# Performance work log

Measured on AMD Instinct MI355X. Metric: run time of the kernel, lower is better.

## Reference

```python
import jax, jax.numpy as jnp
import numpy as np

D = 256       # d_model
H = 8         # nhead
W = 2048      # num windows (single drop level)
T = 64        # max_tokens per window (drop_info['num_sampled_tokens'][dl])
FILL = 48
N = W * FILL  # total voxels


def setup_inputs() -> dict:
    key = jax.random.key(0)
    k0, k1, k2, k3 = jax.random.split(key, 4)
    voxel_feat = jax.random.normal(k0, (N, D), jnp.float32)
    pos_embed = jax.random.normal(k1, (N, D), jnp.float32)
    # nn.MultiheadAttention params: packed in_proj [3D, D] and out_proj [D, D]
    in_proj_w = jax.random.normal(k2, (3 * D, D), jnp.float32) * (1.0 / np.sqrt(D))
    in_proj_b = jnp.zeros((3 * D,), jnp.float32)
    out_proj_w = jax.random.normal(k3, (D, D), jnp.float32) * (1.0 / np.sqrt(D))
    out_proj_b = jnp.zeros((D,), jnp.float32)
    # each voxel assigned a (window, in-window-slot) pair; slots unique per window
    window_idx = (jnp.arange(N) // FILL).astype(jnp.int32)
    slot_idx = (jnp.arange(N) % FILL).astype(jnp.int32)
    return {
        'voxel_feat': voxel_feat, 'pos_embed': pos_embed,
        'in_proj_w': in_proj_w, 'in_proj_b': in_proj_b,
        'out_proj_w': out_proj_w, 'out_proj_b': out_proj_b,
        'window_idx': window_idx, 'slot_idx': slot_idx,
        'num_windows': W, 'max_tokens': T,
    }


def reference(voxel_feat, pos_embed, in_proj_w, in_proj_b, out_proj_w, out_proj_b,
              window_idx, slot_idx, num_windows, max_tokens):
    Dm = voxel_feat.shape[-1]
    hd = Dm // H  # head dim
    P = num_windows * max_tokens  # padded token count
    valid = window_idx.astype(jnp.int32) * max_tokens + slot_idx.astype(jnp.int32)

    # scatter voxels into padded dense windows
    feat = jnp.zeros((P, Dm), voxel_feat.dtype).at[valid].set(voxel_feat)
    pos = jnp.ones((P, Dm), voxel_feat.dtype).at[valid].set(pos_embed)
    kmask = jnp.zeros((P,), bool).at[valid].set(True).reshape(num_windows, max_tokens)  # True = valid key
    feat = feat.reshape(num_windows, max_tokens, Dm)
    pos = pos.reshape(num_windows, max_tokens, Dm)

    # MHA: q = k = feat + pos, v = feat (torch nn.MultiheadAttention math)
    Wq, Wk, Wv = jnp.split(in_proj_w, 3, axis=0)
    bq, bk, bv = jnp.split(in_proj_b, 3, axis=0)
    qk_in = feat + pos
    q = (qk_in @ Wq.T + bq).reshape(num_windows, max_tokens, H, hd)
    k = (qk_in @ Wk.T + bk).reshape(num_windows, max_tokens, H, hd)
    v = (feat @ Wv.T + bv).reshape(num_windows, max_tokens, H, hd)

    scale = 1.0 / np.sqrt(hd)
    scores = jnp.einsum('wqhd,wkhd->whqk', q, k) * scale  # [W, H, T, T]
    scores = jnp.where(kmask[:, None, None, :], scores, -jnp.inf)  # key_padding_mask
    attn = jax.nn.softmax(scores, axis=-1)
    out = jnp.einsum('whqk,wkhd->wqhd', attn, v).reshape(P, Dm)
    out = out @ out_proj_w.T + out_proj_b

    # gather valid tokens back to per-voxel output (padded rows dropped, as in original)
    return out[valid]
```

## Files before the change

kernel.cpp:

```cpp
#include <hip/hip_runtime.h>

#define DD   256
#define HH   8
#define TT   64
#define WW   2048

typedef unsigned short u16;
typedef __attribute__((ext_vector_type(8))) __bf16 bf8_t;
typedef __attribute__((ext_vector_type(4))) float  f32x4;

__device__ __forceinline__ u16 f2bf(float x) {
  union { float f; unsigned u; } c; c.f = x;
  unsigned r = c.u + 0x7FFFu + ((c.u >> 16) & 1u);
  return (u16)(r >> 16);
}
__device__ __forceinline__ float bf2f(u16 x) {
  union { unsigned u; float f; } c; c.u = ((unsigned)x) << 16; return c.f;
}
__device__ __forceinline__ int pack2(float a, float b) {
  return (int)((unsigned)f2bf(a) | ((unsigned)f2bf(b) << 16));
}

__global__ void prep_weights(const float* __restrict__ inw, const float* __restrict__ outw,
                             u16* __restrict__ wq, u16* __restrict__ wo) {
  int i = blockIdx.x * blockDim.x + threadIdx.x;
  if (i < 768 * 256) wq[i] = f2bf(inw[i]);
  if (i < 256 * 256) wo[i] = f2bf(outw[i]);
}

__global__ void build_slots(const int* __restrict__ widx, const int* __restrict__ sidx,
                            int* __restrict__ wslots, int n) {
  int i = blockIdx.x * blockDim.x + threadIdx.x;
  if (i < n) wslots[widx[i] * TT + sidx[i]] = i;
}

__global__ __launch_bounds__(512) void fused_attn(
    const float* __restrict__ feat, const float* __restrict__ pos,
    const u16* __restrict__ wqkv,
    const u16* __restrict__ wout,
    const float* __restrict__ inb, const float* __restrict__ outb,
    const int* __restrict__ wslots, float* __restrict__ out) {

  __shared__ int tl[TT];
  __shared__ u16 bufX[TT * 264];
  __shared__ u16 bufY[DD * 72];

  const int t    = threadIdx.x;
  const int h    = t >> 6;
  const int lane = t & 63;
  const int g    = lane >> 4;
  const int l16  = lane & 15;
  const int w    = blockIdx.x;

  if (t < TT) tl[t] = wslots[w * TT + t];
  __syncthreads();

  const f32x4 zf = {0.f, 0.f, 0.f, 0.f};
  const int stok = t >> 3;
  const int seg  = t & 7;
  const int srow = tl[stok];

  if (srow >= 0) {
    const float4* fp = (const float4*)(feat + (size_t)srow * DD + seg * 32);
    float4 f[8];
#pragma unroll
    for (int j = 0; j < 8; ++j) f[j] = fp[j];
#pragma unroll
    for (int c = 0; c < 4; ++c) {
      union { u16 u[8]; bf8_t v; } r;
#pragma unroll
      for (int j = 0; j < 8; ++j) r.u[j] = f2bf(((const float*)f)[c * 8 + j]);
      *(bf8_t*)&bufX[stok * 264 + seg * 32 + c * 8] = r.v;
    }
  } else {
    union { u16 u[8]; bf8_t v; } z;
#pragma unroll
    for (int j = 0; j < 8; ++j) z.u[j] = 0;
#pragma unroll
    for (int c = 0; c < 4; ++c)
      *(bf8_t*)&bufX[stok * 264 + seg * 32 + c * 8] = z.v;
  }
  __syncthreads();

  f32x4 va[2][4];
#pragma unroll
  for (int md = 0; md < 2; ++md)
#pragma unroll
    for (int nt = 0; nt < 4; ++nt) va[md][nt] = zf;

  for (int kc = 0; kc < 4; ++kc) {
    bf8_t bx[4][2];
#pragma unroll
    for (int nt = 0; nt < 4; ++nt)
#pragma unroll
      for (int ks = 0; ks < 2; ++ks)
        bx[nt][ks] = *(const bf8_t*)&bufX[(nt * 16 + l16) * 264 + kc * 64 + ks * 32 + g * 8];
#pragma unroll
    for (int ks = 0; ks < 2; ++ks) {
      const int kb = kc * 64 + ks * 32 + g * 8;
#pragma unroll
      for (int md = 0; md < 2; ++md) {
        bf8_t awv = *(const bf8_t*)(wqkv + (size_t)(512 + h * 32 + md * 16 + l16) * DD + kb);
#pragma unroll
        for (int nt = 0; nt < 4; ++nt)
          va[md][nt] = __builtin_amdgcn_mfma_f32_16x16x32_bf16(awv, bx[nt][ks], va[md][nt], 0, 0, 0);
      }
    }
  }
  __syncthreads();

  if (srow >= 0) {
    const float4* pp = (const float4*)(pos + (size_t)srow * DD + seg * 32);
    float4 p[8];
#pragma unroll
    for (int j = 0; j < 8; ++j) p[j] = pp[j];
#pragma unroll
    for (int c = 0; c < 4; ++c) {
      union { u16 u[8]; bf8_t v; } xb, r;
      xb.v = *(const bf8_t*)&bufX[stok * 264 + seg * 32 + c * 8];
#pragma unroll
      for (int j = 0; j < 8; ++j)
        r.u[j] = f2bf(bf2f(xb.u[j]) + ((const float*)p)[c * 8 + j]);
      *(bf8_t*)&bufX[stok * 264 + seg * 32 + c * 8] = r.v;
    }
  }
  __syncthreads();

  f32x4 qa[4][2], ka[4][2];
#pragma unroll
  for (int mt = 0; mt < 4; ++mt)
#pragma unroll
    for (int nt = 0; nt < 2; ++nt) { qa[mt][nt] = zf; ka[mt][nt] = zf; }

  for (int kc = 0; kc < 4; ++kc) {
    bf8_t ax[4][2];
#pragma unroll
    for (int mt = 0; mt < 4; ++mt)
#pragma unroll
      for (int ks = 0; ks < 2; ++ks)
        ax[mt][ks] = *(const bf8_t*)&bufX[(mt * 16 + l16) * 264 + kc * 64 + ks * 32 + g * 8];
#pragma unroll
    for (int ks = 0; ks < 2; ++ks) {
      const int kb = kc * 64 + ks * 32 + g * 8;
#pragma unroll
      for (int nt = 0; nt < 2; ++nt) {
        bf8_t bwq = *(const bf8_t*)(wqkv + (size_t)(h * 32 + nt * 16 + l16) * DD + kb);
#pragma unroll
        for (int mt = 0; mt < 4; ++mt)
          qa[mt][nt] = __builtin_amdgcn_mfma_f32_16x16x32_bf16(ax[mt][ks], bwq, qa[mt][nt], 0, 0, 0);
        bf8_t bwk = *(const bf8_t*)(wqkv + (size_t)(256 + h * 32 + nt * 16 + l16) * DD + kb);
#pragma unroll
        for (int mt = 0; mt < 4; ++mt)
          ka[mt][nt] = __builtin_amdgcn_mfma_f32_16x16x32_bf16(ax[mt][ks], bwk, ka[mt][nt], 0, 0, 0);
      }
    }
  }
  __syncthreads();

#pragma unroll
  for (int nt = 0; nt < 2; ++nt) {
    float bq = inb[h * 32 + nt * 16 + l16];
    float bk = inb[256 + h * 32 + nt * 16 + l16];
#pragma unroll
    for (int mt = 0; mt < 4; ++mt)
#pragma unroll
      for (int r = 0; r < 4; ++r) {
        bufX[(mt * 16 + 4 * g + r) * 264 + h * 32 + nt * 16 + l16] = f2bf(qa[mt][nt][r] + bq);
        bufY[(mt * 16 + 4 * g + r) * 264 + h * 32 + nt * 16 + l16] = f2bf(ka[mt][nt][r] + bk);
      }
  }
  __syncthreads();

  bf8_t akf[4], bqf[4];
#pragma unroll
  for (int mt = 0; mt < 4; ++mt) akf[mt] = *(const bf8_t*)&bufY[(mt * 16 + l16) * 264 + h * 32 + g * 8];
#pragma unroll
  for (int nt = 0; nt < 4; ++nt) bqf[nt] = *(const bf8_t*)&bufX[(nt * 16 + l16) * 264 + h * 32 + g * 8];

  f32x4 sa[4][4];
#pragma unroll
  for (int mt = 0; mt < 4; ++mt)
#pragma unroll
    for (int nt = 0; nt < 4; ++nt)
      sa[mt][nt] = __builtin_amdgcn_mfma_f32_16x16x32_bf16(akf[mt], bqf[nt], zf, 0, 0, 0);

  __syncthreads();

#pragma unroll
  for (int md = 0; md < 2; ++md)
#pragma unroll
    for (int r = 0; r < 4; ++r) {
      float bv = inb[512 + h * 32 + md * 16 + 4 * g + r];
#pragma unroll
      for (int nt = 0; nt < 4; ++nt)
        bufY[(h * 32 + md * 16 + 4 * g + r) * 72 + nt * 16 + l16] = f2bf(va[md][nt][r] + bv);
    }

  bool vm[4][4];
#pragma unroll
  for (int mt = 0; mt < 4; ++mt)
#pragma unroll
    for (int r = 0; r < 4; ++r) vm[mt][r] = (tl[mt * 16 + 4 * g + r] >= 0);

  const float scale = 0.17677669529663687f;
  int pk[4][4][2];
#pragma unroll
  for (int nt = 0; nt < 4; ++nt) {
    float sv[4][4];
    float m = -3e38f;
#pragma unroll
    for (int mt = 0; mt < 4; ++mt)
#pragma unroll
      for (int r = 0; r < 4; ++r) {
        float s = vm[mt][r] ? sa[mt][nt][r] * scale : -3e38f;
        sv[mt][r] = s;
        m = fmaxf(m, s);
      }
    m = fmaxf(m, __shfl_xor(m, 16, 64));
    m = fmaxf(m, __shfl_xor(m, 32, 64));
    float sum = 0.f;
#pragma unroll
    for (int mt = 0; mt < 4; ++mt)
#pragma unroll
      for (int r = 0; r < 4; ++r) {
        float p = vm[mt][r] ? __expf(sv[mt][r] - m) : 0.f;
        sv[mt][r] = p;
        sum += p;
      }
    sum += __shfl_xor(sum, 16, 64);
    sum += __shfl_xor(sum, 32, 64);
    float inv = sum > 0.f ? 1.f / sum : 0.f;
#pragma unroll
    for (int mt = 0; mt < 4; ++mt)
#pragma unroll
      for (int rp = 0; rp < 2; ++rp)
        pk[mt][nt][rp] = pack2(sv[mt][2 * rp] * inv, sv[mt][2 * rp + 1] * inv);
  }

  bf8_t avf[2][2];
#pragma unroll
  for (int md = 0; md < 2; ++md)
#pragma unroll
    for (int kk = 0; kk < 2; ++kk)
      avf[md][kk] = *(const bf8_t*)&bufY[(h * 32 + md * 16 + l16) * 72 + kk * 32 + g * 8];

  f32x4 oa[2][4];
#pragma unroll
  for (int md = 0; md < 2; ++md)
#pragma unroll
    for (int nt = 0; nt < 4; ++nt) oa[md][nt] = zf;

#pragma unroll
  for (int kk = 0; kk < 2; ++kk) {
#pragma unroll
    for (int nt = 0; nt < 4; ++nt) {
      union { int wd[4]; bf8_t v; } bu;
#pragma unroll
      for (int wd = 0; wd < 4; ++wd) {
        int src = l16 + 16 * (2 * (g & 1) + (wd >> 1));
        int lo = __shfl(pk[2 * kk + 0][nt][wd & 1], src, 64);
        int hi = __shfl(pk[2 * kk + 1][nt][wd & 1], src, 64);
        bu.wd[wd] = (g & 2) ? hi : lo;
      }
#pragma unroll
      for (int md = 0; md < 2; ++md)
        oa[md][nt] = __builtin_amdgcn_mfma_f32_16x16x32_bf16(avf[md][kk], bu.v, oa[md][nt], 0, 0, 0);
    }
  }

#pragma unroll
  for (int md = 0; md < 2; ++md)
#pragma unroll
    for (int nt = 0; nt < 4; ++nt) {
      union { int wd[2]; } pw;
      pw.wd[0] = pack2(oa[md][nt][0], oa[md][nt][1]);
      pw.wd[1] = pack2(oa[md][nt][2], oa[md][nt][3]);
      *(int2*)&bufX[(nt * 16 + l16) * 264 + h * 32 + md * 16 + 4 * g] = make_int2(pw.wd[0], pw.wd[1]);
    }
  __syncthreads();

  f32x4 fa[4][2];
#pragma unroll
  for (int mt = 0; mt < 4; ++mt)
#pragma unroll
    for (int nt = 0; nt < 2; ++nt) fa[mt][nt] = zf;

#pragma unroll
  for (int kk = 0; kk < 8; ++kk) {
    bf8_t aa[4];
#pragma unroll
    for (int mt = 0; mt < 4; ++mt)
      aa[mt] = *(const bf8_t*)&bufX[(mt * 16 + l16) * 264 + kk * 32 + g * 8];
#pragma unroll
    for (int nt = 0; nt < 2; ++nt) {
      bf8_t bw = *(const bf8_t*)(wout + (size_t)(h * 32 + nt * 16 + l16) * DD + kk * 32 + g * 8);
#pragma unroll
      for (int mt = 0; mt < 4; ++mt)
        fa[mt][nt] = __builtin_amdgcn_mfma_f32_16x16x32_bf16(aa[mt], bw, fa[mt][nt], 0, 0, 0);
    }
  }

#pragma unroll
  for (int nt = 0; nt < 2; ++nt) {
    float ob = outb[h * 32 + nt * 16 + l16];
#pragma unroll
    for (int mt = 0; mt < 4; ++mt)
#pragma unroll
      for (int r = 0; r < 4; ++r) {
        int tok = mt * 16 + 4 * g + r;
        int row = tl[tok];
        if (row >= 0)
          out[(size_t)row * DD + h * 32 + nt * 16 + l16] = fa[mt][nt][r] + ob;
      }
  }
}

extern "C" void kernel_launch(void* const* d_in, const int* in_sizes, int n_in,
                              void* d_out, int out_size, void* d_ws, size_t ws_size,
                              hipStream_t stream) {
  (void)n_in; (void)out_size; (void)ws_size;
  const float* feat = (const float*)d_in[0];
  const float* pos  = (const float*)d_in[1];
  const float* inw  = (const float*)d_in[2];
  const float* inb  = (const float*)d_in[3];
  const float* outw = (const float*)d_in[4];
  const float* outb = (const float*)d_in[5];
  const int*   widx = (const int*)d_in[6];
  const int*   sidx = (const int*)d_in[7];
  const int N = in_sizes[0] / DD;

  char* ws = (char*)d_ws;
  u16* wqkv   = (u16*)ws;
  u16* wout   = (u16*)(ws + 393216);
  int* wslots = (int*)(ws + 393216 + 131072);

  hipMemsetAsync(wslots, 0xFF, WW * TT * sizeof(int), stream);
  prep_weights<<<768, 256, 0, stream>>>(inw, outw, wqkv, wout);
  build_slots<<<(N + 255) / 256, 256, 0, stream>>>(widx, sidx, wslots, N);
  fused_attn<<<WW, 512, 0, stream>>>(feat, pos, wqkv, wout, inb, outb, wslots, (float*)d_out);
}
```

Before: 255.7 us.

## Process eight windows per block with register prefetch of next window's inputs

Each block now loops over eight consecutive windows instead of one. While the current window computes, the next window's feature and position rows and its slot indices are loaded into registers, with double-buffered slot tables in shared memory. Launch bounds are raised to request two blocks per CU. The aim is to hide global-load latency and cut per-block launch overhead. The cost is more register pressure and only 256 blocks, which may under-fill the device's CUs and lengthen the tail.

Result: slower. 324.4 us (+26.8%).

```diff
diff --git a/kernel.cpp b/kernel.cpp
--- a/kernel.cpp
+++ b/kernel.cpp
@@ -4,6 +4,8 @@
 #define HH   8
 #define TT   64
 #define WW   2048
+#define WPB  8
+#define NBLK (WW / WPB)
 
 typedef unsigned short u16;
 typedef __attribute__((ext_vector_type(8))) __bf16 bf8_t;
@@ -34,14 +36,14 @@
   if (i < n) wslots[widx[i] * TT + sidx[i]] = i;
 }
 
-__global__ __launch_bounds__(512) void fused_attn(
+__global__ __launch_bounds__(512, 2) void fused_attn(
     const float* __restrict__ feat, const float* __restrict__ pos,
     const u16* __restrict__ wqkv,
     const u16* __restrict__ wout,
     const float* __restrict__ inb, const float* __restrict__ outb,
     const int* __restrict__ wslots, float* __restrict__ out) {
 
-  __shared__ int tl[TT];
+  __shared__ int tl2[2][TT];
   __shared__ u16 bufX[TT * 264];
   __shared__ u16 bufY[DD * 72];
 
@@ -50,268 +52,292 @@
   const int lane = t & 63;
   const int g    = lane >> 4;
   const int l16  = lane & 15;
-  const int w    = blockIdx.x;
-
-  if (t < TT) tl[t] = wslots[w * TT + t];
+  const int base = blockIdx.x * WPB;
+
+  const int stok  = t >> 3;
+  const int seg   = t & 7;
+  const int tslot = t & 63;
+
+  const f32x4 zf = {0.f, 0.f, 0.f, 0.f};
+
+  int srow_cur = wslots[base * TT + stok];
+  {
+    int tl0 = wslots[base * TT + tslot];
+    if (t < TT) tl2[0][t] = tl0;
+  }
+  float4 fr[8], pr[8];
+  if (srow_cur >= 0) {
+    const float4* fp = (const float4*)(feat + (size_t)srow_cur * DD + seg * 32);
+    const float4* pp = (const float4*)(pos  + (size_t)srow_cur * DD + seg * 32);
+#pragma unroll
+    for (int j = 0; j < 8; ++j) { fr[j] = fp[j]; pr[j] = pp[j]; }
+  }
+  int srowN = wslots[(base + 1) * TT + stok];
+  int tlN   = wslots[(base + 1) * TT + tslot];
   __syncthreads();
 
-  const f32x4 zf = {0.f, 0.f, 0.f, 0.f};
-  const int stok = t >> 3;
-  const int seg  = t & 7;
-  const int srow = tl[stok];
-
-  if (srow >= 0) {
-    const float4* fp = (const float4*)(feat + (size_t)srow * DD + seg * 32);
-    float4 f[8];
-#pragma unroll
-    for (int j = 0; j < 8; ++j) f[j] = fp[j];
-#pragma unroll
-    for (int c = 0; c < 4; ++c) {
-      union { u16 u[8]; bf8_t v; } r;
-#pragma unroll
-      for (int j = 0; j < 8; ++j) r.u[j] = f2bf(((const float*)f)[c * 8 + j]);
-      *(bf8_t*)&bufX[stok * 264 + seg * 32 + c * 8] = r.v;
-    }
-  } else {
-    union { u16 u[8]; bf8_t v; } z;
-#pragma unroll
-    for (int j = 0; j < 8; ++j) z.u[j] = 0;
-#pragma unroll
-    for (int c = 0; c < 4; ++c)
-      *(bf8_t*)&bufX[stok * 264 + seg * 32 + c * 8] = z.v;
-  }
-  __syncthreads();
-
-  f32x4 va[2][4];
-#pragma unroll
-  for (int md = 0; md < 2; ++md)
-#pragma unroll
-    for (int nt = 0; nt < 4; ++nt) va[md][nt] = zf;
-
-  for (int kc = 0; kc < 4; ++kc) {
-    bf8_t bx[4][2];
-#pragma unroll
-    for (int nt = 0; nt < 4; ++nt)
-#pragma unroll
-      for (int ks = 0; ks < 2; ++ks)
-        bx[nt][ks] = *(const bf8_t*)&bufX[(nt * 16 + l16) * 264 + kc * 64 + ks * 32 + g * 8];
-#pragma unroll
-    for (int ks = 0; ks < 2; ++ks) {
-      const int kb = kc * 64 + ks * 32 + g * 8;
-#pragma unroll
-      for (int md = 0; md < 2; ++md) {
-        bf8_t awv = *(const bf8_t*)(wqkv + (size_t)(512 + h * 32 + md * 16 + l16) * DD + kb);
+#pragma unroll 1
+  for (int wi = 0; wi < WPB; ++wi) {
+    const int cb = wi & 1, nb = cb ^ 1;
+
+    if (srow_cur >= 0) {
+#pragma unroll
+      for (int c = 0; c < 4; ++c) {
+        union { u16 u[8]; bf8_t v; } r;
+#pragma unroll
+        for (int j = 0; j < 8; ++j) r.u[j] = f2bf(((const float*)fr)[c * 8 + j]);
+        *(bf8_t*)&bufX[stok * 264 + seg * 32 + c * 8] = r.v;
+      }
+    } else {
+      union { u16 u[8]; bf8_t v; } z;
+#pragma unroll
+      for (int j = 0; j < 8; ++j) z.u[j] = 0;
+#pragma unroll
+      for (int c = 0; c < 4; ++c)
+        *(bf8_t*)&bufX[stok * 264 + seg * 32 + c * 8] = z.v;
+    }
+    if (t < TT && wi + 1 < WPB) tl2[nb][t] = tlN;
+    if (wi + 1 < WPB && srowN >= 0) {
+      const float4* fp = (const float4*)(feat + (size_t)srowN * DD + seg * 32);
+#pragma unroll
+      for (int j = 0; j < 8; ++j) fr[j] = fp[j];
+    }
+    if (wi + 2 < WPB) tlN = wslots[(base + wi + 2) * TT + tslot];
+    __syncthreads();
+
+    f32x4 va[2][4];
+#pragma unroll
+    for (int md = 0; md < 2; ++md)
+#pragma unroll
+      for (int nt = 0; nt < 4; ++nt) va[md][nt] = zf;
+
+    for (int kc = 0; kc < 4; ++kc) {
+      bf8_t bx[4][2];
+#pragma unroll
+      for (int nt = 0; nt < 4; ++nt)
+#pragma unroll
+        for (int ks = 0; ks < 2; ++ks)
+          bx[nt][ks] = *(const bf8_t*)&bufX[(nt * 16 + l16) * 264 + kc * 64 + ks * 32 + g * 8];
+#pragma unroll
+      for (int ks = 0; ks < 2; ++ks) {
+        const int kb = kc * 64 + ks * 32 + g * 8;
+#pragma unroll
+        for (int md = 0; md < 2; ++md) {
+          bf8_t awv = *(const bf8_t*)(wqkv + (size_t)(512 + h * 32 + md * 16 + l16) * DD + kb);
+#pragma unroll
+          for (int nt = 0; nt < 4; ++nt)
+            va[md][nt] = __builtin_amdgcn_mfma_f32_16x16x32_bf16(awv, bx[nt][ks], va[md][nt], 0, 0, 0);
+        }
+      }
+    }
+    __syncthreads();
+
+    if (srow_cur >= 0) {
+#pragma unroll
+      for (int c = 0; c < 4; ++c) {
+        union { u16 u[8]; bf8_t v; } xb, r;
+        xb.v = *(const bf8_t*)&bufX[stok * 264 + seg * 32 + c * 8];
+#pragma unroll
+        for (int j = 0; j < 8; ++j)
+          r.u[j] = f2bf(bf2f(xb.u[j]) + ((const float*)pr)[c * 8 + j]);
+        *(bf8_t*)&bufX[stok * 264 + seg * 32 + c * 8] = r.v;
+      }
+    }
+    if (wi + 1 < WPB && srowN >= 0) {
+      const float4* pp = (const float4*)(pos + (size_t)srowN * DD + seg * 32);
+#pragma unroll
+      for (int j = 0; j < 8; ++j) pr[j] = pp[j];
+    }
+    srow_cur = srowN;
+    if (wi + 2 < WPB) srowN = wslots[(base + wi + 2) * TT + stok];
+    __syncthreads();
+
+    f32x4 qa[4][2], ka[4][2];
+#pragma unroll
+    for (int mt = 0; mt < 4; ++mt)
+#pragma unroll
+      for (int nt = 0; nt < 2; ++nt) { qa[mt][nt] = zf; ka[mt][nt] = zf; }
+
+    for (int kc = 0; kc < 4; ++kc) {
+      bf8_t ax[4][2];
+#pragma unroll
+      for (int mt = 0; mt < 4; ++mt)
+#pragma unroll
+        for (int ks = 0; ks < 2; ++ks)
+          ax[mt][ks] = *(const bf8_t*)&bufX[(mt * 16 + l16) * 264 + kc * 64 + ks * 32 + g * 8];
+#pragma unroll
+      for (int ks = 0; ks < 2; ++ks) {
+        const int kb = kc * 64 + ks * 32 + g * 8;
+#pragma unroll
+        for (int nt = 0; nt < 2; ++nt) {
+          bf8_t bwq = *(const bf8_t*)(wqkv + (size_t)(h * 32 + nt * 16 + l16) * DD + kb);
+#pragma unroll
+          for (int mt = 0; mt < 4; ++mt)
+            qa[mt][nt] = __builtin_amdgcn_mfma_f32_16x16x32_bf16(ax[mt][ks], bwq, qa[mt][nt], 0, 0, 0);
+          bf8_t bwk = *(const bf8_t*)(wqkv + (size_t)(256 + h * 32 + nt * 16 + l16) * DD + kb);
+#pragma unroll
+          for (int mt = 0; mt < 4; ++mt)
+            ka[mt][nt] = __builtin_amdgcn_mfma_f32_16x16x32_bf16(ax[mt][ks], bwk, ka[mt][nt], 0, 0, 0);
+        }
+      }
+    }
+    __syncthreads();
+
+#pragma unroll
+    for (int nt = 0; nt < 2; ++nt) {
+      float bq = inb[h * 32 + nt * 16 + l16];
+      float bk = inb[256 + h * 32 + nt * 16 + l16];
+#pragma unroll
+      for (int mt = 0; mt < 4; ++mt)
+#pragma unroll
+        for (int r = 0; r < 4; ++r) {
+          bufX[(mt * 16 + 4 * g + r) * 264 + h * 32 + nt * 16 + l16] = f2bf(qa[mt][nt][r] + bq);
+          bufY[(mt * 16 + 4 * g + r) * 264 + h * 32 + nt * 16 + l16] = f2bf(ka[mt][nt][r] + bk);
+        }
+    }
+
+    bf8_t akf[4], bqf[4];
+#pragma unroll
+    for (int mt = 0; mt < 4; ++mt) akf[mt] = *(const bf8_t*)&bufY[(mt * 16 + l16) * 264 + h * 32 + g * 8];
+#pragma unroll
+    for (int nt = 0; nt < 4; ++nt) bqf[nt] = *(const bf8_t*)&bufX[(nt * 16 + l16) * 264 + h * 32 + g * 8];
+
+    f32x4 sa[4][4];
+#pragma unroll
+    for (int mt = 0; mt < 4; ++mt)
+#pragma unroll
+      for (int nt = 0; nt < 4; ++nt)
+        sa[mt][nt] = __builtin_amdgcn_mfma_f32_16x16x32_bf16(akf[mt], bqf[nt], zf, 0, 0, 0);
+
+    __syncthreads();
+
+#pragma unroll
+    for (int md = 0; md < 2; ++md)
+#pragma unroll
+      for (int r = 0; r < 4; ++r) {
+        float bv = inb[512 + h * 32 + md * 16 + 4 * g + r];
 #pragma unroll
         for (int nt = 0; nt < 4; ++nt)
-          va[md][nt] = __builtin_amdgcn_mfma_f32_16x16x32_bf16(awv, bx[nt][ks], va[md][nt], 0, 0, 0);
-      }
-    }
-  }
-  __syncthreads();
-
-  if (srow >= 0) {
-    const float4* pp = (const float4*)(pos + (size_t)srow * DD + seg * 32);
-    float4 p[8];
-#pragma unroll
-    for (int j = 0; j < 8; ++j) p[j] = pp[j];
-#pragma unroll
-    for (int c = 0; c < 4; ++c) {
-      union { u16 u[8]; bf8_t v; } xb, r;
-      xb.v = *(const bf8_t*)&bufX[stok * 264 + seg * 32 + c * 8];
-#pragma unroll
-      for (int j = 0; j < 8; ++j)
-        r.u[j] = f2bf(bf2f(xb.u[j]) + ((const float*)p)[c * 8 + j]);
-      *(bf8_t*)&bufX[stok * 264 + seg * 32 + c * 8] = r.v;
-    }
-  }
-  __syncthreads();
-
-  f32x4 qa[4][2], ka[4][2];
-#pragma unroll
-  for (int mt = 0; mt < 4; ++mt)
-#pragma unroll
-    for (int nt = 0; nt < 2; ++nt) { qa[mt][nt] = zf; ka[mt][nt] = zf; }
-
-  for (int kc = 0; kc < 4; ++kc) {
-    bf8_t ax[4][2];
+          bufY[(h * 32 + md * 16 + 4 * g + r) * 72 + nt * 16 + l16] = f2bf(va[md][nt][r] + bv);
+      }
+
+    bool vm[4][4];
 #pragma unroll
     for (int mt = 0; mt < 4; ++mt)
 #pragma unroll
-      for (int ks = 0; ks < 2; ++ks)
-        ax[mt][ks] = *(const bf8_t*)&bufX[(mt * 16 + l16) * 264 + kc * 64 + ks * 32 + g * 8];
-#pragma unroll
-    for (int ks = 0; ks < 2; ++ks) {
-      const int kb = kc * 64 + ks * 32 + g * 8;
+      for (int r = 0; r < 4; ++r) vm[mt][r] = (tl2[cb][mt * 16 + 4 * g + r] >= 0);
+
+    const float scale = 0.17677669529663687f;
+    int pk[4][4][2];
+#pragma unroll
+    for (int nt = 0; nt < 4; ++nt) {
+      float sv[4][4];
+      float m = -3e38f;
+#pragma unroll
+      for (int mt = 0; mt < 4; ++mt)
+#pragma unroll
+        for (int r = 0; r < 4; ++r) {
+          float s = vm[mt][r] ? sa[mt][nt][r] * scale : -3e38f;
+          sv[mt][r] = s;
+          m = fmaxf(m, s);
+        }
+      m = fmaxf(m, __shfl_xor(m, 16, 64));
+      m = fmaxf(m, __shfl_xor(m, 32, 64));
+      float sum = 0.f;
+#pragma unroll
+      for (int mt = 0; mt < 4; ++mt)
+#pragma unroll
+        for (int r = 0; r < 4; ++r) {
+          float p = vm[mt][r] ? __expf(sv[mt][r] - m) : 0.f;
+          sv[mt][r] = p;
+          sum += p;
+        }
+      sum += __shfl_xor(sum, 16, 64);
+      sum += __shfl_xor(sum, 32, 64);
+      float inv = sum > 0.f ? 1.f / sum : 0.f;
+#pragma unroll
+      for (int mt = 0; mt < 4; ++mt)
+#pragma unroll
+        for (int rp = 0; rp < 2; ++rp)
+          pk[mt][nt][rp] = pack2(sv[mt][2 * rp] * inv, sv[mt][2 * rp + 1] * inv);
+    }
+
+    bf8_t avf[2][2];
+#pragma unroll
+    for (int md = 0; md < 2; ++md)
+#pragma unroll
+      for (int kk = 0; kk < 2; ++kk)
+        avf[md][kk] = *(const bf8_t*)&bufY[(h * 32 + md * 16 + l16) * 72 + kk * 32 + g * 8];
+
+    f32x4 oa[2][4];
+#pragma unroll
+    for (int md = 0; md < 2; ++md)
+#pragma unroll
+      for (int nt = 0; nt < 4; ++nt) oa[md][nt] = zf;
+
+#pragma unroll
+    for (int kk = 0; kk < 2; ++kk) {
+#pragma unroll
+      for (int nt = 0; nt < 4; ++nt) {
+        union { int wd[4]; bf8_t v; } bu;
+#pragma unroll
+        for (int wd = 0; wd < 4; ++wd) {
+          int src = l16 + 16 * (2 * (g & 1) + (wd >> 1));
+          int lo = __shfl(pk[2 * kk + 0][nt][wd & 1], src, 64);
+          int hi = __shfl(pk[2 * kk + 1][nt][wd & 1], src, 64);
+          bu.wd[wd] = (g & 2) ? hi : lo;
+        }
+#pragma unroll
+        for (int md = 0; md < 2; ++md)
+          oa[md][nt] = __builtin_amdgcn_mfma_f32_16x16x32_bf16(avf[md][kk], bu.v, oa[md][nt], 0, 0, 0);
+      }
+    }
+
+#pragma unroll
+    for (int md = 0; md < 2; ++md)
+#pragma unroll
+      for (int nt = 0; nt < 4; ++nt) {
+        int w0 = pack2(oa[md][nt][0], oa[md][nt][1]);
+        int w1 = pack2(oa[md][nt][2], oa[md][nt][3]);
+        *(int2*)&bufX[(nt * 16 + l16) * 264 + h * 32 + md * 16 + 4 * g] = make_int2(w0, w1);
+      }
+    __syncthreads();
+
+    f32x4 fa[4][2];
+#pragma unroll
+    for (int mt = 0; mt < 4; ++mt)
+#pragma unroll
+      for (int nt = 0; nt < 2; ++nt) fa[mt][nt] = zf;
+
+#pragma unroll
+    for (int kk = 0; kk < 8; ++kk) {
+      bf8_t aa[4];
+#pragma unroll
+      for (int mt = 0; mt < 4; ++mt)
+        aa[mt] = *(const bf8_t*)&bufX[(mt * 16 + l16) * 264 + kk * 32 + g * 8];
 #pragma unroll
       for (int nt = 0; nt < 2; ++nt) {
-        bf8_t bwq = *(const bf8_t*)(wqkv + (size_t)(h * 32 + nt * 16 + l16) * DD + kb);
+        bf8_t bw = *(const bf8_t*)(wout + (size_t)(h * 32 + nt * 16 + l16) * DD + kk * 32 + g * 8);
 #pragma unroll
         for (int mt = 0; mt < 4; ++mt)
-          qa[mt][nt] = __builtin_amdgcn_mfma_f32_16x16x32_bf16(ax[mt][ks], bwq, qa[mt][nt], 0, 0, 0);
-        bf8_t bwk = *(const bf8_t*)(wqkv + (size_t)(256 + h * 32 + nt * 16 + l16) * DD + kb);
-#pragma unroll
-        for (int mt = 0; mt < 4; ++mt)
-          ka[mt][nt] = __builtin_amdgcn_mfma_f32_16x16x32_bf16(ax[mt][ks], bwk, ka[mt][nt], 0, 0, 0);
-      }
-    }
-  }
-  __syncthreads();
-
-#pragma unroll
-  for (int nt = 0; nt < 2; ++nt) {
-    float bq = inb[h * 32 + nt * 16 + l16];
-    float bk = inb[256 + h * 32 + nt * 16 + l16];
-#pragma unroll
-    for (int mt = 0; mt < 4; ++mt)
-#pragma unroll
-      for (int r = 0; r < 4; ++r) {
-        bufX[(mt * 16 + 4 * g + r) * 264 + h * 32 + nt * 16 + l16] = f2bf(qa[mt][nt][r] + bq);
-        bufY[(mt * 16 + 4 * g + r) * 264 + h * 32 + nt * 16 + l16] = f2bf(ka[mt][nt][r] + bk);
-      }
-  }
-  __syncthreads();
-
-  bf8_t akf[4], bqf[4];
-#pragma unroll
-  for (int mt = 0; mt < 4; ++mt) akf[mt] = *(const bf8_t*)&bufY[(mt * 16 + l16) * 264 + h * 32 + g * 8];
-#pragma unroll
-  for (int nt = 0; nt < 4; ++nt) bqf[nt] = *(const bf8_t*)&bufX[(nt * 16 + l16) * 264 + h * 32 + g * 8];
-
-  f32x4 sa[4][4];
-#pragma unroll
-  for (int mt = 0; mt < 4; ++mt)
-#pragma unroll
-    for (int nt = 0; nt < 4; ++nt)
-      sa[mt][nt] = __builtin_amdgcn_mfma_f32_16x16x32_bf16(akf[mt], bqf[nt], zf, 0, 0, 0);
-
-  __syncthreads();
-
-#pragma unroll
-  for (int md = 0; md < 2; ++md)
-#pragma unroll
-    for (int r = 0; r < 4; ++r) {
-      float bv = inb[512 + h * 32 + md * 16 + 4 * g + r];
-#pragma unroll
-      for (int nt = 0; nt < 4; ++nt)
-        bufY[(h * 32 + md * 16 + 4 * g + r) * 72 + nt * 16 + l16] = f2bf(va[md][nt][r] + bv);
-    }
-
-  bool vm[4][4];
-#pragma unroll
-  for (int mt = 0; mt < 4; ++mt)
-#pragma unroll
-    for (int r = 0; r < 4; ++r) vm[mt][r] = (tl[mt * 16 + 4 * g + r] >= 0);
-
-  const float scale = 0.17677669529663687f;
-  int pk[4][4][2];
-#pragma unroll
-  for (int nt = 0; nt < 4; ++nt) {
-    float sv[4][4];
-    float m = -3e38f;
-#pragma unroll
-    for (int mt = 0; mt < 4; ++mt)
-#pragma unroll
-      for (int r = 0; r < 4; ++r) {
-        float s = vm[mt][r] ? sa[mt][nt][r] * scale : -3e38f;
-        sv[mt][r] = s;
-        m = fmaxf(m, s);
-      }
-    m = fmaxf(m, __shfl_xor(m, 16, 64));
-    m = fmaxf(m, __shfl_xor(m, 32, 64));
-    float sum = 0.f;
-#pragma unroll
-    for (int mt = 0; mt < 4; ++mt)
-#pragma unroll
-      for (int r = 0; r < 4; ++r) {
-        float p = vm[mt][r] ? __expf(sv[mt][r] - m) : 0.f;
-        sv[mt][r] = p;
-        sum += p;
-      }
-    sum += __shfl_xor(sum, 16, 64);
-    sum += __shfl_xor(sum, 32, 64);
-    float inv = sum > 0.f ? 1.f / sum : 0.f;
-#pragma unroll
-    for (int mt = 0; mt < 4; ++mt)
-#pragma unroll
-      for (int rp = 0; rp < 2; ++rp)
-        pk[mt][nt][rp] = pack2(sv[mt][2 * rp] * inv, sv[mt][2 * rp + 1] * inv);
-  }
-
-  bf8_t avf[2][2];
-#pragma unroll
-  for (int md = 0; md < 2; ++md)
-#pragma unroll
-    for (int kk = 0; kk < 2; ++kk)
-      avf[md][kk] = *(const bf8_t*)&bufY[(h * 32 + md * 16 + l16) * 72 + kk * 32 + g * 8];
-
-  f32x4 oa[2][4];
-#pragma unroll
-  for (int md = 0; md < 2; ++md)
-#pragma unroll
-    for (int nt = 0; nt < 4; ++nt) oa[md][nt] = zf;
-
-#pragma unroll
-  for (int kk = 0; kk < 2; ++kk) {
-#pragma unroll
-    for (int nt = 0; nt < 4; ++nt) {
-      union { int wd[4]; bf8_t v; } bu;
-#pragma unroll
-      for (int wd = 0; wd < 4; ++wd) {
-        int src = l16 + 16 * (2 * (g & 1) + (wd >> 1));
-        int lo = __shfl(pk[2 * kk + 0][nt][wd & 1], src, 64);
-        int hi = __shfl(pk[2 * kk + 1][nt][wd & 1], src, 64);
-        bu.wd[wd] = (g & 2) ? hi : lo;
-      }
-#pragma unroll
-      for (int md = 0; md < 2; ++md)
-        oa[md][nt] = __builtin_amdgcn_mfma_f32_16x16x32_bf16(avf[md][kk], bu.v, oa[md][nt], 0, 0, 0);
-    }
-  }
-
-#pragma unroll
-  for (int md = 0; md < 2; ++md)
-#pragma unroll
-    for (int nt = 0; nt < 4; ++nt) {
-      union { int wd[2]; } pw;
-      pw.wd[0] = pack2(oa[md][nt][0], oa[md][nt][1]);
-      pw.wd[1] = pack2(oa[md][nt][2], oa[md][nt][3]);
-      *(int2*)&bufX[(nt * 16 + l16) * 264 + h * 32 + md * 16 + 4 * g] = make_int2(pw.wd[0], pw.wd[1]);
-    }
-  __syncthreads();
-
-  f32x4 fa[4][2];
-#pragma unroll
-  for (int mt = 0; mt < 4; ++mt)
-#pragma unroll
-    for (int nt = 0; nt < 2; ++nt) fa[mt][nt] = zf;
-
-#pragma unroll
-  for (int kk = 0; kk < 8; ++kk) {
-    bf8_t aa[4];
-#pragma unroll
-    for (int mt = 0; mt < 4; ++mt)
-      aa[mt] = *(const bf8_t*)&bufX[(mt * 16 + l16) * 264 + kk * 32 + g * 8];
+          fa[mt][nt] = __builtin_amdgcn_mfma_f32_16x16x32_bf16(aa[mt], bw, fa[mt][nt], 0, 0, 0);
+      }
+    }
+
 #pragma unroll
     for (int nt = 0; nt < 2; ++nt) {
-      bf8_t bw = *(const bf8_t*)(wout + (size_t)(h * 32 + nt * 16 + l16) * DD + kk * 32 + g * 8);
-#pragma unroll
-      for (int mt = 0; mt < 4; ++mt)
-        fa[mt][nt] = __builtin_amdgcn_mfma_f32_16x16x32_bf16(aa[mt], bw, fa[mt][nt], 0, 0, 0);
-    }
-  }
-
-#pragma unroll
-  for (int nt = 0; nt < 2; ++nt) {
-    float ob = outb[h * 32 + nt * 16 + l16];
-#pragma unroll
-    for (int mt = 0; mt < 4; ++mt)
-#pragma unroll
-      for (int r = 0; r < 4; ++r) {
-        int tok = mt * 16 + 4 * g + r;
-        int row = tl[tok];
-        if (row >= 0)
-          out[(size_t)row * DD + h * 32 + nt * 16 + l16] = fa[mt][nt][r] + ob;
-      }
+      float ob = outb[h * 32 + nt * 16 + l16];
+#pragma unroll
+      for (int mt = 0; mt < 4; ++mt)
+#pragma unroll
+        for (int r = 0; r < 4; ++r) {
+          int tok = mt * 16 + 4 * g + r;
+          int row = tl2[cb][tok];
+          if (row >= 0)
+            out[(size_t)row * DD + h * 32 + nt * 16 + l16] = fa[mt][nt][r] + ob;
+        }
+    }
+    __syncthreads();
   }
 }
 
@@ -337,5 +363,5 @@
   hipMemsetAsync(wslots, 0xFF, WW * TT * sizeof(int), stream);
   prep_weights<<<768, 256, 0, stream>>>(inw, outw, wqkv, wout);
   build_slots<<<(N + 255) / 256, 256, 0, stream>>>(widx, sidx, wslots, N);
-  fused_attn<<<WW, 512, 0, stream>>>(feat, pos, wqkv, wout, inb, outb, wslots, (float*)d_out);
-}
+  fused_attn<<<NBLK, 512, 0, stream>>>(feat, pos, wqkv, wout, inb, outb, wslots, (float*)d_out);
+}
```
